# Kernel optimization log

Hardware: AMD Instinct MI355X
Metric: run time of the kernel (lower is better)

## Reference

```python
import jax, jax.numpy as jnp
import numpy as np

N, E, F, H, G = 50000, 1600000, 128, 128, 64
EPS = 1e-5  # BatchNorm eps


def setup_inputs() -> dict:
    key = jax.random.key(0)
    ks = jax.random.split(key, 16)
    x = jax.random.normal(ks[0], (N, F), dtype=jnp.float32)
    edge_index = jax.random.randint(ks[1], (2, E), 0, N, dtype=jnp.int64)
    batch = jnp.sort(jax.random.randint(ks[2], (N,), 0, G, dtype=jnp.int64))
    inp = {
        'x': x, 'edge_index': edge_index, 'batch': batch,
        'W1': jax.random.normal(ks[3], (F, H), dtype=jnp.float32) / np.sqrt(F),
        'b1': jnp.zeros((H,), jnp.float32),
        'bn1_gamma': jax.random.uniform(ks[4], (H,), jnp.float32, 0.5, 1.5),
        'bn1_beta': jax.random.normal(ks[5], (H,), jnp.float32) * 0.1,
        'bn1_mean': jax.random.normal(ks[6], (H,), jnp.float32) * 0.1,
        'bn1_var': jax.random.uniform(ks[7], (H,), jnp.float32, 0.5, 1.5),
        'W2': jax.random.normal(ks[8], (H, H), dtype=jnp.float32) / np.sqrt(H),
        'b2': jnp.zeros((H,), jnp.float32),
        'bn2_gamma': jax.random.uniform(ks[9], (H,), jnp.float32, 0.5, 1.5),
        'bn2_beta': jax.random.normal(ks[10], (H,), jnp.float32) * 0.1,
        'bn2_mean': jax.random.normal(ks[11], (H,), jnp.float32) * 0.1,
        'bn2_var': jax.random.uniform(ks[12], (H,), jnp.float32, 0.5, 1.5),
        'att_w': jax.random.normal(ks[13], (H, 1), dtype=jnp.float32) / np.sqrt(H),
        'cls_w': jax.random.normal(ks[14], (1, H), dtype=jnp.float32) / np.sqrt(H),
        'cls_b': jnp.zeros((1,), jnp.float32),
    }
    return inp


def gcn_conv(h, W, b, src, dst, n):
    # PyG GCNConv: linear, add self-loops, symmetric D^{-1/2}(A+I)D^{-1/2} aggregation, bias.
    hw = h @ W                                   # [n, H]
    loops = jnp.arange(n, dtype=src.dtype)
    s = jnp.concatenate([src, loops])
    d = jnp.concatenate([dst, loops])
    deg = jax.ops.segment_sum(jnp.ones_like(d, dtype=hw.dtype), d, num_segments=n)
    dis = jnp.where(deg > 0, jax.lax.rsqrt(deg), 0.0)
    norm = dis[s] * dis[d]                       # [E+n]
    msgs = hw[s] * norm[:, None]                 # gather + scale (memory-bound)
    return jax.ops.segment_sum(msgs, d, num_segments=n) + b


def batch_norm(h, gamma, beta, mean, var):
    return (h - mean) * gamma * jax.lax.rsqrt(var + EPS) + beta


def reference(x, edge_index, batch, W1, b1, bn1_gamma, bn1_beta, bn1_mean, bn1_var,
              W2, b2, bn2_gamma, bn2_beta, bn2_mean, bn2_var, att_w, cls_w, cls_b):
    n = x.shape[0]
    src, dst = edge_index[0], edge_index[1]
    # eval mode: dropout and edge-dropout are no-ops; BN uses running stats
    h = gcn_conv(x, W1, b1, src, dst, n)
    h = jax.nn.relu(batch_norm(h, bn1_gamma, bn1_beta, bn1_mean, bn1_var))
    h = gcn_conv(h, W2, b2, src, dst, n)
    h = jax.nn.relu(batch_norm(h, bn2_gamma, bn2_beta, bn2_mean, bn2_var))
    att = jax.nn.sigmoid(h @ att_w)              # [n, 1]
    g = jax.ops.segment_sum(h * att, batch, num_segments=G)  # [G, H]
    logits = g @ cls_w.T + cls_b                 # [G, 1]
    return logits, att
```

## Files before the change

kernel.cpp:

```cpp
#include <hip/hip_runtime.h>
#include <math.h>

#define NN 50000
#define HID 128
#define NG 64
#define BN_EPS 1e-5f

typedef __attribute__((ext_vector_type(8))) short short8;
typedef __attribute__((ext_vector_type(4))) float f32x4;
typedef __attribute__((ext_vector_type(2))) float f32x2;

__device__ inline unsigned pack_bf2(float a, float b) {
    union { float f; unsigned u; } ua, ub;
    ua.f = a; ub.f = b;
    unsigned x = ua.u, y = ub.u;
    x += 0x7fffu + ((x >> 16) & 1u);
    y += 0x7fffu + ((y >> 16) & 1u);
    return (x >> 16) | (y & 0xffff0000u);
}
__device__ inline unsigned short bf16_1(float x) {
    union { float f; unsigned u; } v;
    v.f = x;
    unsigned r = v.u + 0x7fffu + ((v.u >> 16) & 1u);
    return (unsigned short)(r >> 16);
}
__device__ inline float2 unpack_bf2(unsigned v) {
    union { unsigned u; float f; } a, b;
    a.u = v << 16;
    b.u = v & 0xffff0000u;
    return make_float2(a.f, b.f);
}
__device__ __forceinline__ f32x2 bf2_to_f32x2(unsigned u) {
    union { unsigned q; float f; } a, b;
    a.q = u << 16;
    b.q = u & 0xffff0000u;
    f32x2 r;
    r.x = a.f;
    r.y = b.f;
    return r;
}

#define NBKT 256
#define ETILE 4096
#define EPT   (ETILE / 256)
#define CAPB  10240
#define CAPC  12800
#define ASTR 136

__global__ __launch_bounds__(128) void k_prep0(const float* __restrict__ W1,
                                               const float* __restrict__ W2,
                                               unsigned short* __restrict__ wt1,
                                               unsigned short* __restrict__ wt2,
                                               int* __restrict__ bcurP,
                                               const float* __restrict__ cls_b,
                                               float* __restrict__ logits,
                                               unsigned short* __restrict__ zb,
                                               unsigned short* __restrict__ hwsb2,
                                               int n) {
    int b = blockIdx.x;
    int t = threadIdx.x;
    if (b < 256) {
        int k = b & 127;
        const float* W = (b < 128) ? W1 : W2;
        unsigned short* wt = (b < 128) ? wt1 : wt2;
        wt[t * 128 + k] = bf16_1(W[k * 128 + t]);
    } else {
        #pragma unroll
        for (int i = 0; i < 32; ++i) bcurP[t * 32 + i] = 0;
        if (t < NG) logits[t] = cls_b[0];
        if (t < 64) *(unsigned*)((char*)zb + (size_t)n * 256 + t * 4) = 0u;
        else        *(unsigned*)((char*)hwsb2 + (size_t)n * 256 + (t - 64) * 4) = 0u;
    }
}

__device__ __forceinline__ void gemm1_tile(char* smem, int row0,
                                           const float* __restrict__ x,
                                           const unsigned short* __restrict__ wt1,
                                           unsigned short* __restrict__ zb,
                                           int n, int t) {
    typedef unsigned short ArowT[ASTR];
    ArowT* A = (ArowT*)smem;
    #pragma unroll
    for (int i = 0; i < 8; ++i) {
        int idx = t + i * 256;
        int r = idx >> 5;
        int c4 = (idx & 31) * 4;
        float4 v = make_float4(0.f, 0.f, 0.f, 0.f);
        if (row0 + r < n) v = *(const float4*)&x[(size_t)(row0 + r) * 128 + c4];
        uint2 p;
        p.x = pack_bf2(v.x, v.y);
        p.y = pack_bf2(v.z, v.w);
        *(uint2*)&A[r][c4] = p;
    }
    __syncthreads();
    int lane = t & 63;
    int wave = t >> 6;
    int m = lane & 15;
    int quad = lane >> 4;
    int r0 = wave * 16;
    short8 a[4];
    #pragma unroll
    for (int kt = 0; kt < 4; ++kt)
        a[kt] = *(const short8*)&A[r0 + m][kt * 32 + quad * 8];
    f32x4 acc[8];
    #pragma unroll
    for (int ct = 0; ct < 8; ++ct) acc[ct] = (f32x4){0.f, 0.f, 0.f, 0.f};
    short8 bcur[4], bnxt[4];
    {
        const unsigned short* wb = &wt1[(size_t)m * 128 + quad * 8];
        #pragma unroll
        for (int kt = 0; kt < 4; ++kt) bcur[kt] = *(const short8*)(wb + kt * 32);
    }
    #pragma unroll
    for (int ct = 0; ct < 8; ++ct) {
        if (ct < 7) {
            const unsigned short* wb = &wt1[(size_t)((ct + 1) * 16 + m) * 128 + quad * 8];
            #pragma unroll
            for (int kt = 0; kt < 4; ++kt) bnxt[kt] = *(const short8*)(wb + kt * 32);
        }
        #pragma unroll
        for (int kt = 0; kt < 4; ++kt)
            acc[ct] = __builtin_amdgcn_mfma_f32_16x16x32_bf16(a[kt], bcur[kt], acc[ct], 0, 0, 0);
        #pragma unroll
        for (int kt = 0; kt < 4; ++kt) bcur[kt] = bnxt[kt];
    }
    __syncthreads();
    #pragma unroll
    for (int ct = 0; ct < 8; ++ct) {
        int col = ct * 16 + m;
        #pragma unroll
        for (int reg = 0; reg < 4; ++reg)
            A[r0 + quad * 4 + reg][col] = bf16_1(acc[ct][reg]);
    }
    __syncthreads();
    #pragma unroll
    for (int i = 0; i < 4; ++i) {
        int idx = t + i * 256;
        int r = idx >> 4;
        int c8 = (idx & 15) * 8;
        int grow = row0 + r;
        if (grow < n)
            *(uint4*)&zb[(size_t)grow * 128 + c8] = *(const uint4*)&A[r][c8];
    }
}

struct SmemDist {
    int h[NBKT], sx[NBKT], cur[NBKT], gb[NBKT];
    unsigned stage[ETILE];
};

__global__ __launch_bounds__(256) void k_dist_gemm1(const int* __restrict__ src,
                                                    const int* __restrict__ dst,
                                                    int* __restrict__ bcurP,
                                                    unsigned* __restrict__ bpacked,
                                                    const float* __restrict__ x,
                                                    const unsigned short* __restrict__ wt1,
                                                    unsigned short* __restrict__ zb,
                                                    int E, int n, int DB) {
    __shared__ __align__(16) char smem[sizeof(SmemDist)];
    int t = threadIdx.x;
    int b = blockIdx.x;

    if (b >= DB) {
        gemm1_tile(smem, (b - DB) * 64, x, wt1, zb, n, t);
        return;
    }
    SmemDist* s = (SmemDist*)smem;
    s->h[t] = 0;
    __syncthreads();
    int base = b * ETILE;
    int dreg[EPT];
    #pragma unroll
    for (int i = 0; i < EPT; ++i) {
        int e = base + i * 256 + t;
        dreg[i] = (e < E) ? dst[e] : -1;
        if (dreg[i] >= 0) atomicAdd(&s->h[dreg[i] >> 8], 1);
    }
    __syncthreads();
    int c = s->h[t];
    s->sx[t] = c;
    __syncthreads();
    for (int off = 1; off < NBKT; off <<= 1) {
        int v = (t >= off) ? s->sx[t - off] : 0;
        __syncthreads();
        s->sx[t] += v;
        __syncthreads();
    }
    int nvalid = s->sx[NBKT - 1];
    int excl = s->sx[t] - c;
    __syncthreads();
    s->sx[t] = excl;
    s->cur[t] = excl;
    s->gb[t] = (c > 0) ? atomicAdd(&bcurP[t * 16], c) : 0;
    __syncthreads();
    #pragma unroll
    for (int i = 0; i < EPT; ++i) {
        int e = base + i * 256 + t;
        if (dreg[i] >= 0) {
            int d = dreg[i];
            int bkt = d >> 8;
            int p = atomicAdd(&s->cur[bkt], 1);
            s->stage[p] = ((unsigned)d << 16) | (unsigned)src[e];
        }
    }
    __syncthreads();
    for (int idx = t; idx < nvalid; idx += 256) {
        unsigned v = s->stage[idx];
        int bkt = (int)(v >> 24);
        int pos = s->gb[bkt] + (idx - s->sx[bkt]);
        bpacked[(size_t)bkt * CAPB + pos] = v;
    }
}

struct SmemCSR {
    int cnt[NBKT], sA[NBKT], cur[NBKT];
    unsigned short stage[CAPC];
};

__global__ __launch_bounds__(256) void k_csr_gemm1(const unsigned* __restrict__ bpacked,
                                                   const int* __restrict__ bcurP,
                                                   int* __restrict__ row_ptr,
                                                   int* __restrict__ degA,
                                                   float* __restrict__ dis,
                                                   unsigned short* __restrict__ col16,
                                                   const float* __restrict__ x,
                                                   const unsigned short* __restrict__ wt1,
                                                   unsigned short* __restrict__ zb,
                                                   int n, int NB, int row0B) {
    __shared__ __align__(16) char smem[sizeof(SmemCSR)];
    int t = threadIdx.x;
    int b = blockIdx.x;

    if (b >= NB) {
        gemm1_tile(smem, row0B + (b - NB) * 64, x, wt1, zb, n, t);
        return;
    }
    SmemCSR* s = (SmemCSR*)smem;
    int node0 = b << 8;
    int nn = n - node0;
    if (nn > 256) nn = 256;
    if (nn < 0) nn = 0;
    int e0 = b * CAPB;
    int e0c = b * CAPC;
    int ne = bcurP[b * 16];
    s->cnt[t] = 0;
    __syncthreads();
    int n4 = (ne + 3) >> 2;
    for (int i = t; i < n4; i += 256) {
        uint4 v = *(const uint4*)&bpacked[e0 + 4 * i];
        int rem = ne - 4 * i;
        if (rem > 0) atomicAdd(&s->cnt[(v.x >> 16) & 255u], 1);
        if (rem > 1) atomicAdd(&s->cnt[(v.y >> 16) & 255u], 1);
        if (rem > 2) atomicAdd(&s->cnt[(v.z >> 16) & 255u], 1);
        if (rem > 3) atomicAdd(&s->cnt[(v.w >> 16) & 255u], 1);
    }
    __syncthreads();
    int c = s->cnt[t];
    int gm = max(c, __shfl_xor(c, 1));
    gm = max(gm, __shfl_xor(gm, 2));
    int P = (gm + 7) & ~7;
    s->sA[t] = P;
    __syncthreads();
    for (int off = 1; off < NBKT; off <<= 1) {
        int v = (t >= off) ? s->sA[t - off] : 0;
        __syncthreads();
        s->sA[t] += v;
        __syncthreads();
    }
    int excl = s->sA[t] - P;
    s->cur[t] = excl;
    if (t < nn) {
        row_ptr[node0 + t] = e0c + excl;
        degA[node0 + t] = P;
        dis[node0 + t] = rsqrtf((float)(c + 1));
    }
    __syncthreads();
    int totP = s->sA[NBKT - 1];
    unsigned short sent = (unsigned short)n;
    for (int i = t; i < totP; i += 256) s->stage[i] = sent;
    __syncthreads();
    for (int i = t; i < n4; i += 256) {
        uint4 v = *(const uint4*)&bpacked[e0 + 4 * i];
        int rem = ne - 4 * i;
        unsigned vv[4] = {v.x, v.y, v.z, v.w};
        #pragma unroll
        for (int j = 0; j < 4; ++j) {
            if (rem > j) {
                int ld = (int)((vv[j] >> 16) & 255u);
                int p = atomicAdd(&s->cur[ld], 1);
                s->stage[p] = (unsigned short)(vv[j] & 0xFFFFu);
            }
        }
    }
    __syncthreads();
    int nw = totP >> 1;
    for (int i = t; i < nw; i += 256) {
        unsigned w = (unsigned)s->stage[2 * i] | ((unsigned)s->stage[2 * i + 1] << 16);
        *(unsigned*)&col16[e0c + 2 * i] = w;
    }
}

__global__ __launch_bounds__(256) void k_scale(unsigned short* __restrict__ zb,
                                               const float* __restrict__ dis, int n) {
    int i = blockIdx.x * 256 + threadIdx.x;
    int r = i >> 4;
    if (r >= n) return;
    int c8 = (i & 15) * 8;
    float s = dis[r];
    uint4 v = *(const uint4*)&zb[(size_t)r * 128 + c8];
    unsigned* w = (unsigned*)&v;
    #pragma unroll
    for (int k = 0; k < 4; ++k) {
        float2 f = unpack_bf2(w[k]);
        w[k] = pack_bf2(f.x * s, f.y * s);
    }
    *(uint4*)&zb[(size_t)r * 128 + c8] = v;
}


__device__ __forceinline__ void consume8(const uint4* v, f32x2* acc) {
    #pragma unroll
    for (int j = 0; j < 8; ++j) {
        const unsigned* w = (const unsigned*)&v[j];
        #pragma unroll
        for (int i2 = 0; i2 < 4; ++i2)
            acc[i2] += bf2_to_f32x2(w[i2]);
    }
}

__device__ __forceinline__ void issue8(const unsigned short* __restrict__ hws,
                                       int sl, int lsel, int creg, uint4* v) {
    #pragma unroll
    for (int j = 0; j < 8; ++j) {
        int s = __shfl(creg, lsel + j);
        v[j] = *(const uint4*)(hws + ((size_t)s << 7) + (sl << 3));
    }
}

__device__ __forceinline__ void gather_pipe(const unsigned short* __restrict__ hws,
                                            const unsigned short* __restrict__ col16,
                                            int e0, int P, int sl, int part,
                                            f32x2* acc) {
    int nt = P >> 3;
    if (nt <= 0) return;
    int base = part << 4;
    uint4 vA[8], vB[8];
    int c0 = (int)col16[e0 + sl];
    int c1 = (int)col16[e0 + 16 + sl];
    int n0 = 0, n1 = 0;

    issue8(hws, sl, base, c0, vA);
    int t = 0, ebase = 0;
    for (;;) {
        if (t + 4 < nt) {
            n0 = (int)col16[e0 + ebase + 32 + sl];
            n1 = (int)col16[e0 + ebase + 48 + sl];
        }
        if (t + 1 < nt) issue8(hws, sl, base + 8, c0, vB);
        consume8(vA, acc);
        if (++t >= nt) break;
        if (t + 1 < nt) issue8(hws, sl, base, c1, vA);
        consume8(vB, acc);
        if (++t >= nt) break;
        if (t + 1 < nt) issue8(hws, sl, base + 8, c1, vB);
        consume8(vA, acc);
        if (++t >= nt) break;
        if (t + 1 < nt) issue8(hws, sl, base, n0, vA);
        consume8(vB, acc);
        if (++t >= nt) break;
        c0 = n0; c1 = n1; ebase += 32;
    }
}


__global__ __launch_bounds__(256, 3) void k_agg1_gemm2(const unsigned short* __restrict__ zb,
                                                       const int* __restrict__ row_ptr,
                                                       const int* __restrict__ degA,
                                                       const unsigned short* __restrict__ col16,
                                                       const float* __restrict__ dis,
                                                       const float* __restrict__ bias,
                                                       const float* __restrict__ gamma,
                                                       const float* __restrict__ beta,
                                                       const float* __restrict__ mean,
                                                       const float* __restrict__ var,
                                                       const unsigned short* __restrict__ wt2,
                                                       unsigned short* __restrict__ hwsb2, int n) {
    __shared__ unsigned short H1[16][ASTR];
    __shared__ unsigned short C2[16][ASTR];
    int t = threadIdx.x;
    int wave = t >> 6, lane = t & 63;
    int sl = lane & 15, part = lane >> 4;
    int d = blockIdx.x * 16 + wave * 4 + part;
    bool active = (d < n);
    int e0 = 0, P = 0;
    if (active) {
        e0 = row_ptr[d];
        P = degA[d];
    }
    uint4 vs = make_uint4(0, 0, 0, 0);
    float dd = 0.f;
    if (active) {
        vs = *(const uint4*)(zb + ((size_t)d << 7) + (sl << 3));
        dd = dis[d];
    }
    int md = P;
    md = max(md, __shfl_xor(md, 16));
    md = max(md, __shfl_xor(md, 32));

    f32x2 acc[4];
    #pragma unroll
    for (int i = 0; i < 4; ++i) acc[i] = (f32x2){0.f, 0.f};
    gather_pipe(zb, col16, e0, md, sl, part, acc);

    unsigned outw[4] = {0, 0, 0, 0};
    if (active) {
        const unsigned* w = (const unsigned*)&vs;
        #pragma unroll
        for (int i2 = 0; i2 < 4; ++i2)
            acc[i2] += bf2_to_f32x2(w[i2]);
        int f0 = sl << 3;
        #pragma unroll
        for (int i2 = 0; i2 < 4; ++i2) {
            int f = f0 + 2 * i2;
            float2 bv = *(const float2*)&bias[f];
            float2 gm = *(const float2*)&gamma[f];
            float2 bt = *(const float2*)&beta[f];
            float2 mn = *(const float2*)&mean[f];
            float2 vr = *(const float2*)&var[f];
            float vx = acc[i2].x * dd + bv.x;
            float vy = acc[i2].y * dd + bv.y;
            float sx = gm.x * rsqrtf(vr.x + BN_EPS);
            float sy = gm.y * rsqrtf(vr.y + BN_EPS);
            float rx = fmaxf((vx - mn.x) * sx + bt.x, 0.f);
            float ry = fmaxf((vy - mn.y) * sy + bt.y, 0.f);
            outw[i2] = pack_bf2(rx, ry);
        }
    }
    int local = wave * 4 + part;
    *(uint4*)&H1[local][sl << 3] = *(uint4*)outw;
    __syncthreads();

    int m = sl;
    int quad = part;
    short8 a2[4];
    #pragma unroll
    for (int kt = 0; kt < 4; ++kt)
        a2[kt] = *(const short8*)&H1[m][kt * 32 + quad * 8];

    f32x4 acc2[2];
    acc2[0] = (f32x4){0.f, 0.f, 0.f, 0.f};
    acc2[1] = (f32x4){0.f, 0.f, 0.f, 0.f};
    #pragma unroll
    for (int i = 0; i < 2; ++i) {
        int ct = wave * 2 + i;
        const unsigned short* wb = &wt2[(size_t)(ct * 16 + m) * 128 + quad * 8];
        #pragma unroll
        for (int kt = 0; kt < 4; ++kt) {
            short8 b = *(const short8*)(wb + kt * 32);
            acc2[i] = __builtin_amdgcn_mfma_f32_16x16x32_bf16(a2[kt], b, acc2[i], 0, 0, 0);
        }
    }
    int gr = blockIdx.x * 16 + quad * 4;
    float ds2[4];
    #pragma unroll
    for (int reg = 0; reg < 4; ++reg)
        ds2[reg] = (gr + reg < n) ? dis[gr + reg] : 0.f;
    #pragma unroll
    for (int i = 0; i < 2; ++i) {
        int col = (wave * 2 + i) * 16 + m;
        #pragma unroll
        for (int reg = 0; reg < 4; ++reg)
            C2[quad * 4 + reg][col] = bf16_1(acc2[i][reg] * ds2[reg]);
    }
    __syncthreads();
    {
        int r = t >> 4;
        int c8 = (t & 15) * 8;
        int grow = blockIdx.x * 16 + r;
        if (grow < n)
            *(uint4*)&hwsb2[(size_t)grow * 128 + c8] = *(const uint4*)&C2[r][c8];
    }
}


__global__ __launch_bounds__(256, 3) void k_agg2_att_logit(const unsigned short* __restrict__ hwsb,
                                                           const int* __restrict__ row_ptr,
                                                           const int* __restrict__ degA,
                                                           const unsigned short* __restrict__ col16,
                                                           const float* __restrict__ dis,
                                                           const float* __restrict__ bias,
                                                           const float* __restrict__ gamma,
                                                           const float* __restrict__ beta,
                                                           const float* __restrict__ mean,
                                                           const float* __restrict__ var,
                                                           const int* __restrict__ batch,
                                                           const float* __restrict__ att_w,
                                                           const float* __restrict__ cls_w,
                                                           float* __restrict__ att_out,
                                                           float* __restrict__ logits, int n) {
    __shared__ int   sg[16];
    __shared__ float sv[16];
    int t = threadIdx.x;
    int wave = t >> 6, lane = t & 63;
    int sl = lane & 15, part = lane >> 4;
    int d = blockIdx.x * 16 + wave * 4 + part;
    bool active = (d < n);
    int e0 = 0, P = 0;
    if (active) {
        e0 = row_ptr[d];
        P = degA[d];
    }
    uint4 vs = make_uint4(0, 0, 0, 0);
    float dd = 0.f;
    int g = -1;
    if (active) {
        vs = *(const uint4*)(hwsb + ((size_t)d << 7) + (sl << 3));
        dd = dis[d];
        g = batch[d];
    }
    int md = P;
    md = max(md, __shfl_xor(md, 16));
    md = max(md, __shfl_xor(md, 32));

    f32x2 acc[4];
    #pragma unroll
    for (int i = 0; i < 4; ++i) acc[i] = (f32x2){0.f, 0.f};
    gather_pipe(hwsb, col16, e0, md, sl, part, acc);

    float contrib = 0.f;
    float p = 0.f, q = 0.f;
    if (active) {
        const unsigned* w = (const unsigned*)&vs;
        #pragma unroll
        for (int i2 = 0; i2 < 4; ++i2)
            acc[i2] += bf2_to_f32x2(w[i2]);
        float dd2 = dd;
        int f0 = sl << 3;
        #pragma unroll
        for (int i2 = 0; i2 < 4; ++i2) {
            int f = f0 + 2 * i2;
            float2 bv = *(const float2*)&bias[f];
            float2 gm = *(const float2*)&gamma[f];
            float2 bt = *(const float2*)&beta[f];
            float2 mn = *(const float2*)&mean[f];
            float2 vr = *(const float2*)&var[f];
            float vx = acc[i2].x * dd2 + bv.x;
            float vy = acc[i2].y * dd2 + bv.y;
            float sx = gm.x * rsqrtf(vr.x + BN_EPS);
            float sy = gm.y * rsqrtf(vr.y + BN_EPS);
            float rx = fmaxf((vx - mn.x) * sx + bt.x, 0.f);
            float ry = fmaxf((vy - mn.y) * sy + bt.y, 0.f);
            float2 aw = *(const float2*)&att_w[f];
            float2 cw = *(const float2*)&cls_w[f];
            p += rx * aw.x + ry * aw.y;
            q += rx * cw.x + ry * cw.y;
        }
    }
    #pragma unroll
    for (int off = 1; off < 16; off <<= 1) {
        p += __shfl_xor(p, off);
        q += __shfl_xor(q, off);
    }
    if (active) {
        float a = 1.f / (1.f + expf(-p));
        if (sl == 0) att_out[d] = a;
        contrib = a * q;
    }
    if (sl == 0) {
        sg[wave * 4 + part] = g;
        sv[wave * 4 + part] = contrib;
    }
    __syncthreads();
    if (t == 0) {
        int cur = -1;
        float acc2 = 0.f;
        #pragma unroll
        for (int i = 0; i < 16; ++i) {
            int gi = sg[i];
            if (gi < 0) continue;
            if (gi != cur) {
                if (cur >= 0) atomicAdd(&logits[cur], acc2);
                cur = gi;
                acc2 = 0.f;
            }
            acc2 += sv[i];
        }
        if (cur >= 0) atomicAdd(&logits[cur], acc2);
    }
}


extern "C" void kernel_launch(void* const* d_in, const int* in_sizes, int n_in,
                              void* d_out, int out_size, void* d_ws, size_t ws_size,
                              hipStream_t stream) {
    const float* x   = (const float*)d_in[0];
    const int*   ei  = (const int*)d_in[1];
    const int*   bat = (const int*)d_in[2];
    const float* W1  = (const float*)d_in[3];
    const float* b1  = (const float*)d_in[4];
    const float* g1  = (const float*)d_in[5];
    const float* bt1 = (const float*)d_in[6];
    const float* mn1 = (const float*)d_in[7];
    const float* vr1 = (const float*)d_in[8];
    const float* W2  = (const float*)d_in[9];
    const float* b2  = (const float*)d_in[10];
    const float* g2  = (const float*)d_in[11];
    const float* bt2 = (const float*)d_in[12];
    const float* mn2 = (const float*)d_in[13];
    const float* vr2 = (const float*)d_in[14];
    const float* attw = (const float*)d_in[15];
    const float* clsw = (const float*)d_in[16];
    const float* clsb = (const float*)d_in[17];

    int E = in_sizes[1] / 2;
    int n = in_sizes[2];
    const int* src = ei;
    const int* dst = ei + E;
    int NB = (n + 255) >> 8;

    char* ws = (char*)d_ws;
    auto alloc = [&](size_t bytes) {
        void* p = (void*)ws;
        ws += (bytes + 255) & ~(size_t)255;
        return p;
    };
    int*            bcurP   = (int*)alloc(NBKT * 16 * 4);
    unsigned*       bpacked = (unsigned*)alloc((size_t)NBKT * CAPB * 4);
    int*            row_ptr = (int*)alloc((size_t)n * 4);
    int*            degA    = (int*)alloc((size_t)n * 4);
    unsigned short* col16   = (unsigned short*)alloc(((size_t)NBKT * CAPC + 1024) * 2);
    float*          dis     = (float*)alloc((size_t)n * 4);
    unsigned short* zb      = (unsigned short*)alloc((size_t)(n + 1) * 128 * 2);
    unsigned short* hwsb2   = (unsigned short*)alloc((size_t)(n + 1) * 128 * 2);
    unsigned short* wt1     = (unsigned short*)alloc(128 * 128 * 2);
    unsigned short* wt2     = (unsigned short*)alloc(128 * 128 * 2);

    float* out = (float*)d_out;
    int DB = (E + ETILE - 1) / ETILE;
    int gb = (n + 63) / 64;
    int G1A = gb / 2;
    int G1B = gb - G1A;
    int ab = (n + 15) / 16;
    int sb = (n * 16 + 255) / 256;

    k_prep0<<<257, 128, 0, stream>>>(W1, W2, wt1, wt2, bcurP, clsb, out, zb, hwsb2, n);
    k_dist_gemm1<<<DB + G1A, 256, 0, stream>>>(src, dst, bcurP, bpacked, x, wt1, zb,
                                               E, n, DB);
    k_csr_gemm1<<<NB + G1B, 256, 0, stream>>>(bpacked, bcurP, row_ptr, degA, dis,
                                              col16, x, wt1, zb, n, NB, G1A * 64);
    k_scale<<<sb, 256, 0, stream>>>(zb, dis, n);
    k_agg1_gemm2<<<ab, 256, 0, stream>>>(zb, row_ptr, degA, col16, dis,
                                         b1, g1, bt1, mn1, vr1, wt2, hwsb2, n);
    k_agg2_att_logit<<<ab, 256, 0, stream>>>(hwsb2, row_ptr, degA, col16, dis,
                                             b2, g2, bt2, mn2, vr2, bat, attw, clsw,
                                             out + NG, out, n);
}
```

Baseline: 255.3 us.

## Fuse degree scaling into CSR kernel and move all GEMM1 tiles to dist kernel

All GEMM1 row tiles now run alongside the edge distribution kernel instead of being split across two launches. The CSR build kernel applies the per-node D^-1/2 scaling to zb directly from shared-memory degrees, so the separate scale kernel is removed. The weight transpose in prep now goes through shared memory with coalesced accesses in 3 blocks instead of 257. The intent is fewer launches and one fewer pass over zb, at the cost of a longer critical path in the first kernel and extra tail work in the CSR blocks.

Measured after the change: 254.4 us. About the same (-0.4%).

```diff
diff --git a/kernel.cpp b/kernel.cpp
--- a/kernel.cpp
+++ b/kernel.cpp
@@ -47,7 +47,7 @@
 #define CAPC  12800
 #define ASTR 136
 
-__global__ __launch_bounds__(128) void k_prep0(const float* __restrict__ W1,
+__global__ __launch_bounds__(256) void k_prep0(const float* __restrict__ W1,
                                                const float* __restrict__ W2,
                                                unsigned short* __restrict__ wt1,
                                                unsigned short* __restrict__ wt2,
@@ -59,17 +59,30 @@
                                                int n) {
     int b = blockIdx.x;
     int t = threadIdx.x;
-    if (b < 256) {
-        int k = b & 127;
-        const float* W = (b < 128) ? W1 : W2;
-        unsigned short* wt = (b < 128) ? wt1 : wt2;
-        wt[t * 128 + k] = bf16_1(W[k * 128 + t]);
+    if (b < 2) {
+        __shared__ unsigned short T[128][130];
+        const float* W = b ? W2 : W1;
+        unsigned short* wt = b ? wt2 : wt1;
+        #pragma unroll
+        for (int i = 0; i < 64; ++i) {
+            int idx = i * 256 + t;
+            int r = idx >> 7, c = idx & 127;
+            T[c][r] = bf16_1(W[r * 128 + c]);
+        }
+        __syncthreads();
+        #pragma unroll
+        for (int i = 0; i < 32; ++i) {
+            int idx = i * 256 + t;
+            int r = idx >> 6, c2 = (idx & 63) * 2;
+            unsigned w = (unsigned)T[r][c2] | ((unsigned)T[r][c2 + 1] << 16);
+            *(unsigned*)&wt[r * 128 + c2] = w;
+        }
     } else {
         #pragma unroll
-        for (int i = 0; i < 32; ++i) bcurP[t * 32 + i] = 0;
+        for (int i = 0; i < 16; ++i) bcurP[t * 16 + i] = 0;
         if (t < NG) logits[t] = cls_b[0];
         if (t < 64) *(unsigned*)((char*)zb + (size_t)n * 256 + t * 4) = 0u;
-        else        *(unsigned*)((char*)hwsb2 + (size_t)n * 256 + (t - 64) * 4) = 0u;
+        else if (t < 128) *(unsigned*)((char*)hwsb2 + (size_t)n * 256 + (t - 64) * 4) = 0u;
     }
 }
 
@@ -214,28 +227,22 @@
 
 struct SmemCSR {
     int cnt[NBKT], sA[NBKT], cur[NBKT];
+    float disL[NBKT];
     unsigned short stage[CAPC];
 };
 
-__global__ __launch_bounds__(256) void k_csr_gemm1(const unsigned* __restrict__ bpacked,
+__global__ __launch_bounds__(256) void k_csr_scale(const unsigned* __restrict__ bpacked,
                                                    const int* __restrict__ bcurP,
                                                    int* __restrict__ row_ptr,
                                                    int* __restrict__ degA,
                                                    float* __restrict__ dis,
                                                    unsigned short* __restrict__ col16,
-                                                   const float* __restrict__ x,
-                                                   const unsigned short* __restrict__ wt1,
                                                    unsigned short* __restrict__ zb,
-                                                   int n, int NB, int row0B) {
-    __shared__ __align__(16) char smem[sizeof(SmemCSR)];
+                                                   int n) {
+    __shared__ __align__(16) char smemc[sizeof(SmemCSR)];
+    SmemCSR* s = (SmemCSR*)smemc;
     int t = threadIdx.x;
     int b = blockIdx.x;
-
-    if (b >= NB) {
-        gemm1_tile(smem, row0B + (b - NB) * 64, x, wt1, zb, n, t);
-        return;
-    }
-    SmemCSR* s = (SmemCSR*)smem;
     int node0 = b << 8;
     int nn = n - node0;
     if (nn > 256) nn = 256;
@@ -269,10 +276,12 @@
     }
     int excl = s->sA[t] - P;
     s->cur[t] = excl;
+    float dv = rsqrtf((float)(c + 1));
+    s->disL[t] = dv;
     if (t < nn) {
         row_ptr[node0 + t] = e0c + excl;
         degA[node0 + t] = P;
-        dis[node0 + t] = rsqrtf((float)(c + 1));
+        dis[node0 + t] = dv;
     }
     __syncthreads();
     int totP = s->sA[NBKT - 1];
@@ -298,23 +307,20 @@
         unsigned w = (unsigned)s->stage[2 * i] | ((unsigned)s->stage[2 * i + 1] << 16);
         *(unsigned*)&col16[e0c + 2 * i] = w;
     }
-}
-
-__global__ __launch_bounds__(256) void k_scale(unsigned short* __restrict__ zb,
-                                               const float* __restrict__ dis, int n) {
-    int i = blockIdx.x * 256 + threadIdx.x;
-    int r = i >> 4;
-    if (r >= n) return;
-    int c8 = (i & 15) * 8;
-    float s = dis[r];
-    uint4 v = *(const uint4*)&zb[(size_t)r * 128 + c8];
-    unsigned* w = (unsigned*)&v;
-    #pragma unroll
-    for (int k = 0; k < 4; ++k) {
-        float2 f = unpack_bf2(w[k]);
-        w[k] = pack_bf2(f.x * s, f.y * s);
-    }
-    *(uint4*)&zb[(size_t)r * 128 + c8] = v;
+    for (int idx = t; idx < nn * 16; idx += 256) {
+        int r = idx >> 4;
+        int c8 = (idx & 15) * 8;
+        float sc = s->disL[r];
+        size_t o8 = (size_t)(node0 + r) * 128 + c8;
+        uint4 v = *(const uint4*)&zb[o8];
+        unsigned* w = (unsigned*)&v;
+        #pragma unroll
+        for (int k2 = 0; k2 < 4; ++k2) {
+            float2 f = unpack_bf2(w[k2]);
+            w[k2] = pack_bf2(f.x * sc, f.y * sc);
+        }
+        *(uint4*)&zb[o8] = v;
+    }
 }
 
 
@@ -638,17 +644,13 @@
     float* out = (float*)d_out;
     int DB = (E + ETILE - 1) / ETILE;
     int gb = (n + 63) / 64;
-    int G1A = gb / 2;
-    int G1B = gb - G1A;
     int ab = (n + 15) / 16;
-    int sb = (n * 16 + 255) / 256;
-
-    k_prep0<<<257, 128, 0, stream>>>(W1, W2, wt1, wt2, bcurP, clsb, out, zb, hwsb2, n);
-    k_dist_gemm1<<<DB + G1A, 256, 0, stream>>>(src, dst, bcurP, bpacked, x, wt1, zb,
-                                               E, n, DB);
-    k_csr_gemm1<<<NB + G1B, 256, 0, stream>>>(bpacked, bcurP, row_ptr, degA, dis,
-                                              col16, x, wt1, zb, n, NB, G1A * 64);
-    k_scale<<<sb, 256, 0, stream>>>(zb, dis, n);
+
+    k_prep0<<<3, 256, 0, stream>>>(W1, W2, wt1, wt2, bcurP, clsb, out, zb, hwsb2, n);
+    k_dist_gemm1<<<DB + gb, 256, 0, stream>>>(src, dst, bcurP, bpacked, x, wt1, zb,
+                                              E, n, DB);
+    k_csr_scale<<<NB, 256, 0, stream>>>(bpacked, bcurP, row_ptr, degA, dis,
+                                        col16, zb, n);
     k_agg1_gemm2<<<ab, 256, 0, stream>>>(zb, row_ptr, degA, col16, dis,
                                          b1, g1, bt1, mn1, vr1, wt2, hwsb2, n);
     k_agg2_att_logit<<<ab, 256, 0, stream>>>(hwsb2, row_ptr, degA, col16, dis,
```
